# Optimization experiments

Hardware: AMD Instinct MI355X
Metric: run time of the kernel (lower is better)

The kernel has to match this reference:

```python
import jax, jax.numpy as jnp
import numpy as np

POOL_VOLUME = 8  # prod(pool_size) = 2*2*2 for dimension=3

N_IN = 1500000
N_OUT = 375000
C = 64

def setup_inputs() -> dict:
    key = jax.random.key(0)
    k1, k2, k3 = jax.random.split(key, 3)
    input_features = jax.random.normal(k1, (N_IN, C), dtype=jnp.float32)
    # Rulebook: (input_row, output_row) pairs; with pool=stride=2 each active
    # input site contributes to exactly one output site.
    rules_in = jax.random.randint(k2, (N_IN,), 0, N_IN, dtype=jnp.int32)
    rules_out = jax.random.randint(k3, (N_IN,), 0, N_OUT, dtype=jnp.int32)
    return {
        "input_features": input_features,
        "rules_in": rules_in,
        "rules_out": rules_out,
        "n_out": N_OUT,
    }

def reference(input_features, rules_in, rules_out, n_out):
    # Sparse average pooling: gather active input rows per rulebook entry,
    # segment-sum into output sites, normalize by the fixed filter volume
    # (SCN AveragePooling divides by prod(pool_size), not active count).
    gathered = input_features[rules_in] * (1.0 / POOL_VOLUME)  # [n_rules, C]
    out = jax.ops.segment_sum(gathered, rules_out, num_segments=n_out)  # [n_out, C]
    return out
```

## Files before the change

kernel.cpp:

```cpp
#include <hip/hip_runtime.h>
#include <hip/hip_bf16.h>


#define C_CHANNELS 64
#define CAP 24
#define OVF_CAP 16384

__global__ __launch_bounds__(256) void
zero_ws_kernel(int4* __restrict__ cnt4, int n4, int* __restrict__ ovf_cnt) {
    int i = blockIdx.x * blockDim.x + threadIdx.x;
    if (i < n4) cnt4[i] = make_int4(0, 0, 0, 0);
    if (i == 0) *ovf_cnt = 0;
}

__global__ __launch_bounds__(256) void
build_kernel(const int* __restrict__ rules_in,
             const int* __restrict__ rules_out,
             int* __restrict__ cnt,
             int* __restrict__ list,
             int* __restrict__ ovf_cnt,
             int2* __restrict__ ovf_pairs,
             int n_rules) {
    int r = blockIdx.x * blockDim.x + threadIdx.x;
    if (r >= n_rules) return;
    int ro = rules_out[r];
    int ri = rules_in[r];
    int pos = atomicAdd(&cnt[ro], 1);
    if (pos < CAP) {
        list[(size_t)ro * CAP + pos] = ri;
    } else {
        int oi = atomicAdd(ovf_cnt, 1);
        if (oi < OVF_CAP) ovf_pairs[oi] = make_int2(ri, ro);
    }
}

__global__ __launch_bounds__(256) void
gather_kernel(const float* __restrict__ in,
              const int* __restrict__ cnt,
              const int* __restrict__ list,
              float* __restrict__ out,
              int n_out) {
    int idx = blockIdx.x * blockDim.x + threadIdx.x;
    int ro = idx >> 4;
    int c4 = (idx & 15) << 2;
    if (ro >= n_out) return;

    int count = cnt[ro];
    int k = count < CAP ? count : CAP;
    const int* lp = list + (size_t)ro * CAP;

    float4 s = {0.f, 0.f, 0.f, 0.f};
    int j = 0;
    for (; j + 4 <= k; j += 4) {
        int4 r4 = *reinterpret_cast<const int4*>(lp + j);
        float4 v0 = *reinterpret_cast<const float4*>(in + (size_t)r4.x * C_CHANNELS + c4);
        float4 v1 = *reinterpret_cast<const float4*>(in + (size_t)r4.y * C_CHANNELS + c4);
        float4 v2 = *reinterpret_cast<const float4*>(in + (size_t)r4.z * C_CHANNELS + c4);
        float4 v3 = *reinterpret_cast<const float4*>(in + (size_t)r4.w * C_CHANNELS + c4);
        s.x += (v0.x + v1.x) + (v2.x + v3.x);
        s.y += (v0.y + v1.y) + (v2.y + v3.y);
        s.z += (v0.z + v1.z) + (v2.z + v3.z);
        s.w += (v0.w + v1.w) + (v2.w + v3.w);
    }
    for (; j < k; ++j) {
        int row = lp[j];
        float4 v = *reinterpret_cast<const float4*>(in + (size_t)row * C_CHANNELS + c4);
        s.x += v.x; s.y += v.y; s.z += v.z; s.w += v.w;
    }

    float4 o = {s.x * 0.125f, s.y * 0.125f, s.z * 0.125f, s.w * 0.125f};
    *reinterpret_cast<float4*>(out + (size_t)ro * C_CHANNELS + c4) = o;
}

__global__ __launch_bounds__(256) void
ovf_scatter_kernel(const float* __restrict__ in,
                   const int* __restrict__ ovf_cnt,
                   const int2* __restrict__ ovf_pairs,
                   float* __restrict__ out) {
    int idx = blockIdx.x * blockDim.x + threadIdx.x;
    int p  = idx >> 4;
    int c4 = (idx & 15) << 2;
    int n = *ovf_cnt;
    if (n > OVF_CAP) n = OVF_CAP;
    if (p >= n) return;
    int2 pr = ovf_pairs[p];
    const float4 v = *reinterpret_cast<const float4*>(
        in + (size_t)pr.x * C_CHANNELS + c4);
    float* o = out + (size_t)pr.y * C_CHANNELS + c4;
    atomicAdd(o + 0, v.x * 0.125f);
    atomicAdd(o + 1, v.y * 0.125f);
    atomicAdd(o + 2, v.z * 0.125f);
    atomicAdd(o + 3, v.w * 0.125f);
}

__global__ __launch_bounds__(256) void
zero4_kernel(float4* __restrict__ p, long n4) {
    long i = (long)blockIdx.x * blockDim.x + threadIdx.x;
    long stride = (long)gridDim.x * blockDim.x;
    float4 z = {0.f, 0.f, 0.f, 0.f};
    for (; i < n4; i += stride) p[i] = z;
}

__global__ __launch_bounds__(256) void
avgpool_scatter_kernel(const float* __restrict__ in,
                       const int* __restrict__ rules_in,
                       const int* __restrict__ rules_out,
                       float* __restrict__ out,
                       int n_rules) {
    int idx = blockIdx.x * blockDim.x + threadIdx.x;
    int rule = idx >> 4;
    int c4   = (idx & 15) << 2;
    if (rule >= n_rules) return;
    int ri = rules_in[rule];
    int ro = rules_out[rule];
    const float4 v = *reinterpret_cast<const float4*>(
        in + (size_t)ri * C_CHANNELS + c4);
    float* o = out + (size_t)ro * C_CHANNELS + c4;
    atomicAdd(o + 0, v.x * 0.125f);
    atomicAdd(o + 1, v.y * 0.125f);
    atomicAdd(o + 2, v.z * 0.125f);
    atomicAdd(o + 3, v.w * 0.125f);
}

extern "C" void kernel_launch(void* const* d_in, const int* in_sizes, int n_in,
                              void* d_out, int out_size, void* d_ws, size_t ws_size,
                              hipStream_t stream) {
    const float* in        = (const float*)d_in[0];
    const int*   rules_in  = (const int*)d_in[1];
    const int*   rules_out = (const int*)d_in[2];
    float*       out       = (float*)d_out;

    const int n_rules = in_sizes[1];
    const int n_out   = out_size / C_CHANNELS;

    size_t cnt_bytes  = (size_t)n_out * sizeof(int);
    size_t cnt_pad    = (cnt_bytes + 15) & ~(size_t)15;
    size_t list_bytes = (size_t)n_out * CAP * sizeof(int);
    size_t list_pad   = (list_bytes + 15) & ~(size_t)15;
    size_t ovf_hdr    = 16;
    size_t need = cnt_pad + list_pad + ovf_hdr + (size_t)OVF_CAP * sizeof(int2);

    const int block = 256;

    if (ws_size < need) {
        long n4 = (long)out_size / 4;
        int grid = (int)((n4 + block - 1) / block);
        if (grid > 65535) grid = 65535;
        zero4_kernel<<<grid, block, 0, stream>>>((float4*)out, n4);
        int total = n_rules * 16;
        avgpool_scatter_kernel<<<(total + block - 1) / block, block, 0, stream>>>(
            in, rules_in, rules_out, out, n_rules);
        return;
    }

    int*  cnt       = (int*)d_ws;
    int*  list      = (int*)((char*)d_ws + cnt_pad);
    int*  ovf_cnt   = (int*)((char*)d_ws + cnt_pad + list_pad);
    int2* ovf_pairs = (int2*)((char*)d_ws + cnt_pad + list_pad + ovf_hdr);

    {
        int n4 = n_out / 4;
        zero_ws_kernel<<<(n4 + block - 1) / block, block, 0, stream>>>(
            (int4*)cnt, n4, ovf_cnt);
    }

    build_kernel<<<(n_rules + block - 1) / block, block, 0, stream>>>(
        rules_in, rules_out, cnt, list, ovf_cnt, ovf_pairs, n_rules);

    {
        long total = (long)n_out * 16;
        int grid = (int)((total + block - 1) / block);
        gather_kernel<<<grid, block, 0, stream>>>(in, cnt, list, out, n_out);
    }

    {
        int total = OVF_CAP * 16;
        ovf_scatter_kernel<<<total / block, block, 0, stream>>>(
            in, ovf_cnt, ovf_pairs, out);
    }
}
```

Baseline: 665.5 us.

## Colocate per-output count and index list in one 64-byte bucket row

Merges the separate count array and per-output index list into a single 16-int row per output, with the count in slot 0 and up to 15 indices after it. Both the build atomics and the gather lookup then touch one cache line per output. The build kernel handles four rules per thread with vector loads. The gather uses an unrolled branchy accumulation and nontemporal stores, and the overflow kernel becomes grid-stride with a fixed grid. The cost is zeroing a much larger workspace and a lower per-bucket capacity before falling back to atomics.

```diff
diff --git a/kernel.cpp b/kernel.cpp
--- a/kernel.cpp
+++ b/kernel.cpp
@@ -1,43 +1,63 @@
 #include <hip/hip_runtime.h>
-#include <hip/hip_bf16.h>
 
 
 #define C_CHANNELS 64
-#define CAP 24
+#define ROW_INTS 16
+#define CAP_ENT 15
 #define OVF_CAP 16384
 
-__global__ __launch_bounds__(256) void
-zero_ws_kernel(int4* __restrict__ cnt4, int n4, int* __restrict__ ovf_cnt) {
+typedef float f32x4 __attribute__((ext_vector_type(4)));
+
+__global__ __launch_bounds__(256) void
+zero_ws_kernel(int4* __restrict__ p, int n4, int* __restrict__ ovf_cnt) {
     int i = blockIdx.x * blockDim.x + threadIdx.x;
-    if (i < n4) cnt4[i] = make_int4(0, 0, 0, 0);
-    if (i == 0) *ovf_cnt = 0;
+    int stride = gridDim.x * blockDim.x;
+    int4 z = make_int4(0, 0, 0, 0);
+    for (; i < n4; i += stride) p[i] = z;
+    if (blockIdx.x == 0 && threadIdx.x == 0) *ovf_cnt = 0;
+}
+
+__device__ __forceinline__ void
+push_rule(int ri, int ro,
+          int* __restrict__ bucket,
+          int* __restrict__ ovf_cnt,
+          int2* __restrict__ ovf_pairs) {
+    int* row = bucket + (size_t)ro * ROW_INTS;
+    int pos = atomicAdd(row, 1);
+    if (pos < CAP_ENT) {
+        row[1 + pos] = ri;
+    } else {
+        int oi = atomicAdd(ovf_cnt, 1);
+        if (oi < OVF_CAP) ovf_pairs[oi] = make_int2(ri, ro);
+    }
 }
 
 __global__ __launch_bounds__(256) void
 build_kernel(const int* __restrict__ rules_in,
              const int* __restrict__ rules_out,
-             int* __restrict__ cnt,
-             int* __restrict__ list,
+             int* __restrict__ bucket,
              int* __restrict__ ovf_cnt,
              int2* __restrict__ ovf_pairs,
              int n_rules) {
-    int r = blockIdx.x * blockDim.x + threadIdx.x;
-    if (r >= n_rules) return;
-    int ro = rules_out[r];
-    int ri = rules_in[r];
-    int pos = atomicAdd(&cnt[ro], 1);
-    if (pos < CAP) {
-        list[(size_t)ro * CAP + pos] = ri;
+    int t = blockIdx.x * blockDim.x + threadIdx.x;
+    int r0 = t << 2;
+    if (r0 >= n_rules) return;
+    if (r0 + 4 <= n_rules) {
+        int4 ri4 = *reinterpret_cast<const int4*>(rules_in + r0);
+        int4 ro4 = *reinterpret_cast<const int4*>(rules_out + r0);
+        push_rule(ri4.x, ro4.x, bucket, ovf_cnt, ovf_pairs);
+        push_rule(ri4.y, ro4.y, bucket, ovf_cnt, ovf_pairs);
+        push_rule(ri4.z, ro4.z, bucket, ovf_cnt, ovf_pairs);
+        push_rule(ri4.w, ro4.w, bucket, ovf_cnt, ovf_pairs);
     } else {
-        int oi = atomicAdd(ovf_cnt, 1);
-        if (oi < OVF_CAP) ovf_pairs[oi] = make_int2(ri, ro);
+        for (int r = r0; r < n_rules; ++r)
+            push_rule(rules_in[r], rules_out[r], bucket, ovf_cnt, ovf_pairs);
     }
 }
 
 __global__ __launch_bounds__(256) void
 gather_kernel(const float* __restrict__ in,
-              const int* __restrict__ cnt,
-              const int* __restrict__ list,
+              const int* __restrict__ bucket,
               float* __restrict__ out,
               int n_out) {
     int idx = blockIdx.x * blockDim.x + threadIdx.x;
@@ -45,31 +65,44 @@
     int c4 = (idx & 15) << 2;
     if (ro >= n_out) return;
 
-    int count = cnt[ro];
-    int k = count < CAP ? count : CAP;
-    const int* lp = list + (size_t)ro * CAP;
-
-    float4 s = {0.f, 0.f, 0.f, 0.f};
-    int j = 0;
-    for (; j + 4 <= k; j += 4) {
-        int4 r4 = *reinterpret_cast<const int4*>(lp + j);
-        float4 v0 = *reinterpret_cast<const float4*>(in + (size_t)r4.x * C_CHANNELS + c4);
-        float4 v1 = *reinterpret_cast<const float4*>(in + (size_t)r4.y * C_CHANNELS + c4);
-        float4 v2 = *reinterpret_cast<const float4*>(in + (size_t)r4.z * C_CHANNELS + c4);
-        float4 v3 = *reinterpret_cast<const float4*>(in + (size_t)r4.w * C_CHANNELS + c4);
-        s.x += (v0.x + v1.x) + (v2.x + v3.x);
-        s.y += (v0.y + v1.y) + (v2.y + v3.y);
-        s.z += (v0.z + v1.z) + (v2.z + v3.z);
-        s.w += (v0.w + v1.w) + (v2.w + v3.w);
-    }
-    for (; j < k; ++j) {
-        int row = lp[j];
-        float4 v = *reinterpret_cast<const float4*>(in + (size_t)row * C_CHANNELS + c4);
-        s.x += v.x; s.y += v.y; s.z += v.z; s.w += v.w;
-    }
-
-    float4 o = {s.x * 0.125f, s.y * 0.125f, s.z * 0.125f, s.w * 0.125f};
-    *reinterpret_cast<float4*>(out + (size_t)ro * C_CHANNELS + c4) = o;
+    const int4* row = reinterpret_cast<const int4*>(bucket + (size_t)ro * ROW_INTS);
+    int4 q0 = row[0];
+    int4 q1 = row[1];
+    int k = q0.x < CAP_ENT ? q0.x : CAP_ENT;
+
+    f32x4 s = {0.f, 0.f, 0.f, 0.f};
+
+#define ACC(ridx) \
+    s += *reinterpret_cast<const f32x4*>(in + (size_t)(unsigned)(ridx) * C_CHANNELS + c4)
+
+    if (k > 0) {
+        ACC(q0.y);
+        if (k > 1)  ACC(q0.z);
+        if (k > 2)  ACC(q0.w);
+        if (k > 3)  ACC(q1.x);
+        if (k > 4)  ACC(q1.y);
+        if (k > 5)  ACC(q1.z);
+        if (k > 6)  ACC(q1.w);
+        if (k > 7) {
+            int4 q2 = row[2];
+            ACC(q2.x);
+            if (k > 8)  ACC(q2.y);
+            if (k > 9)  ACC(q2.z);
+            if (k > 10) ACC(q2.w);
+            if (k > 11) {
+                int4 q3 = row[3];
+                ACC(q3.x);
+                if (k > 12) ACC(q3.y);
+                if (k > 13) ACC(q3.z);
+                if (k > 14) ACC(q3.w);
+            }
+        }
+    }
+#undef ACC
+
+    f32x4 o = s * 0.125f;
+    __builtin_nontemporal_store(
+        o, reinterpret_cast<f32x4*>(out + (size_t)ro * C_CHANNELS + c4));
 }
 
 __global__ __launch_bounds__(256) void
@@ -77,20 +110,22 @@
                    const int* __restrict__ ovf_cnt,
                    const int2* __restrict__ ovf_pairs,
                    float* __restrict__ out) {
-    int idx = blockIdx.x * blockDim.x + threadIdx.x;
-    int p  = idx >> 4;
-    int c4 = (idx & 15) << 2;
     int n = *ovf_cnt;
     if (n > OVF_CAP) n = OVF_CAP;
-    if (p >= n) return;
-    int2 pr = ovf_pairs[p];
-    const float4 v = *reinterpret_cast<const float4*>(
-        in + (size_t)pr.x * C_CHANNELS + c4);
-    float* o = out + (size_t)pr.y * C_CHANNELS + c4;
-    atomicAdd(o + 0, v.x * 0.125f);
-    atomicAdd(o + 1, v.y * 0.125f);
-    atomicAdd(o + 2, v.z * 0.125f);
-    atomicAdd(o + 3, v.w * 0.125f);
+    int total = n * 16;
+    int stride = gridDim.x * blockDim.x;
+    for (int idx = blockIdx.x * blockDim.x + threadIdx.x; idx < total; idx += stride) {
+        int p  = idx >> 4;
+        int c4 = (idx & 15) << 2;
+        int2 pr = ovf_pairs[p];
+        const float4 v = *reinterpret_cast<const float4*>(
+            in + (size_t)pr.x * C_CHANNELS + c4);
+        float* o = out + (size_t)pr.y * C_CHANNELS + c4;
+        atomicAdd(o + 0, v.x * 0.125f);
+        atomicAdd(o + 1, v.y * 0.125f);
+        atomicAdd(o + 2, v.z * 0.125f);
+        atomicAdd(o + 3, v.w * 0.125f);
+    }
 }
 
 __global__ __launch_bounds__(256) void
@@ -133,12 +168,10 @@
     const int n_rules = in_sizes[1];
     const int n_out   = out_size / C_CHANNELS;
 
-    size_t cnt_bytes  = (size_t)n_out * sizeof(int);
-    size_t cnt_pad    = (cnt_bytes + 15) & ~(size_t)15;
-    size_t list_bytes = (size_t)n_out * CAP * sizeof(int);
+    size_t list_bytes = (size_t)n_out * ROW_INTS * sizeof(int);
     size_t list_pad   = (list_bytes + 15) & ~(size_t)15;
     size_t ovf_hdr    = 16;
-    size_t need = cnt_pad + list_pad + ovf_hdr + (size_t)OVF_CAP * sizeof(int2);
+    size_t need = list_pad + ovf_hdr + (size_t)OVF_CAP * sizeof(int2);
 
     const int block = 256;
 
@@ -153,29 +186,27 @@
         return;
     }
 
-    int*  cnt       = (int*)d_ws;
-    int*  list      = (int*)((char*)d_ws + cnt_pad);
-    int*  ovf_cnt   = (int*)((char*)d_ws + cnt_pad + list_pad);
-    int2* ovf_pairs = (int2*)((char*)d_ws + cnt_pad + list_pad + ovf_hdr);
+    int*  bucket    = (int*)d_ws;
+    int*  ovf_cnt   = (int*)((char*)d_ws + list_pad);
+    int2* ovf_pairs = (int2*)((char*)d_ws + list_pad + ovf_hdr);
 
     {
-        int n4 = n_out / 4;
-        zero_ws_kernel<<<(n4 + block - 1) / block, block, 0, stream>>>(
-            (int4*)cnt, n4, ovf_cnt);
-    }
-
-    build_kernel<<<(n_rules + block - 1) / block, block, 0, stream>>>(
-        rules_in, rules_out, cnt, list, ovf_cnt, ovf_pairs, n_rules);
+        int n4 = (int)(list_bytes / 16);
+        int grid = (n4 + block - 1) / block;
+        zero_ws_kernel<<<grid, block, 0, stream>>>((int4*)bucket, n4, ovf_cnt);
+    }
+
+    {
+        int threads = (n_rules + 3) / 4;
+        build_kernel<<<(threads + block - 1) / block, block, 0, stream>>>(
+            rules_in, rules_out, bucket, ovf_cnt, ovf_pairs, n_rules);
+    }
 
     {
         long total = (long)n_out * 16;
         int grid = (int)((total + block - 1) / block);
-        gather_kernel<<<grid, block, 0, stream>>>(in, cnt, list, out, n_out);
-    }
-
-    {
-        int total = OVF_CAP * 16;
-        ovf_scatter_kernel<<<total / block, block, 0, stream>>>(
-            in, ovf_cnt, ovf_pairs, out);
-    }
-}
+        gather_kernel<<<grid, block, 0, stream>>>(in, bucket, out, n_out);
+    }
+
+    ovf_scatter_kernel<<<64, block, 0, stream>>>(in, ovf_cnt, ovf_pairs, out);
+}
```

Result: faster. 602.7 us (-9.4%).
